# Optimization experiments

Hardware: AMD Instinct MI355X
Metric: run time of the kernel (lower is better)

## Reference

```python
import jax, jax.numpy as jnp
import numpy as np

N_NODES = 20000
N_EDGES = 640000
HIDDEN = 128
NUM_FILTERS = 128
NUM_RBF = 50
NUM_LAYERS = 6
MAX_Z = 100
CUTOFF_UPPER = 5.0
CUTOFF_LOWER = 0.0


def _cosine_cutoff(d):
    # torchmd CosineCutoff with cutoff_lower == 0
    c = 0.5 * (jnp.cos(d * jnp.pi / CUTOFF_UPPER) + 1.0)
    return c * (d < CUTOFF_UPPER).astype(d.dtype)


def setup_inputs() -> dict:
    key = jax.random.key(0)
    ks = jax.random.split(key, 16)
    s = 0.05
    z = jax.random.randint(ks[0], (N_NODES,), 0, MAX_Z)
    pos = jax.random.uniform(ks[1], (N_NODES, 3), dtype=jnp.float32) * 3.0
    src = jax.random.randint(ks[2], (N_EDGES,), 0, N_NODES)
    off = jax.random.randint(ks[3], (N_EDGES,), 1, N_NODES)
    dst = (src + off) % N_NODES  # no self loops -> d > 0 a.s.
    edge_index = jnp.stack([src, dst])
    batch = jnp.zeros((N_NODES,), dtype=jnp.int32)
    # expnorm RBF initial params (ExpNormalSmearing._initial_params)
    start = float(np.exp(-CUTOFF_UPPER + CUTOFF_LOWER))
    rbf_means = jnp.linspace(start, 1.0, NUM_RBF, dtype=jnp.float32)
    rbf_betas = jnp.full((NUM_RBF,), (2.0 / NUM_RBF * (1.0 - start)) ** -2, dtype=jnp.float32)

    def w(k, shape):
        return jax.random.normal(k, shape, dtype=jnp.float32) * s

    L = NUM_LAYERS
    return dict(
        z=z, pos=pos, edge_index=edge_index, batch=batch,
        emb_table=w(ks[4], (MAX_Z, HIDDEN)),
        nbr_emb_table=w(ks[5], (MAX_Z, HIDDEN)),
        nbr_proj_W=w(ks[6], (NUM_RBF, HIDDEN)),
        nbr_proj_b=jnp.zeros((HIDDEN,), jnp.float32),
        combine_W=w(ks[7], (2 * HIDDEN, HIDDEN)),
        combine_b=jnp.zeros((HIDDEN,), jnp.float32),
        rbf_means=rbf_means, rbf_betas=rbf_betas,
        mlp_W1=w(ks[8], (L, NUM_RBF, NUM_FILTERS)),
        mlp_b1=jnp.zeros((L, NUM_FILTERS), jnp.float32),
        mlp_W2=w(ks[9], (L, NUM_FILTERS, NUM_FILTERS)),
        mlp_b2=jnp.zeros((L, NUM_FILTERS), jnp.float32),
        lin1_W=w(ks[10], (L, HIDDEN, NUM_FILTERS)),
        lin2_W=w(ks[11], (L, NUM_FILTERS, HIDDEN)),
        lin2_b=jnp.zeros((L, HIDDEN), jnp.float32),
        lin_W=w(ks[12], (L, HIDDEN, HIDDEN)),
        lin_b=jnp.zeros((L, HIDDEN), jnp.float32),
    )


def reference(z, pos, edge_index, batch, emb_table, nbr_emb_table,
              nbr_proj_W, nbr_proj_b, combine_W, combine_b,
              rbf_means, rbf_betas,
              mlp_W1, mlp_b1, mlp_W2, mlp_b2,
              lin1_W, lin2_W, lin2_b, lin_W, lin_b):
    src, dst = edge_index[0], edge_index[1]
    # Distance (loop=False): edge_vec = pos[src] - pos[dst]
    vec = pos[src] - pos[dst]                      # [E, 3]
    d = jnp.sqrt(jnp.sum(vec * vec, axis=-1))      # [E]
    C = _cosine_cutoff(d)                          # [E]
    alpha = 5.0 / (CUTOFF_UPPER - CUTOFF_LOWER)
    # ExpNormalSmearing: C(d) * exp(-beta * (exp(alpha*(-d+low)) - mu)^2)
    edge_attr = C[:, None] * jnp.exp(
        -rbf_betas * (jnp.exp(alpha * (-d[:, None] + CUTOFF_LOWER)) - rbf_means) ** 2
    )                                              # [E, R]
    x = emb_table[z]                               # [N, H]
    # NeighborEmbedding (self-loop edges masked out, add aggregation)
    nl_mask = (src != dst).astype(x.dtype)
    Wn = (edge_attr @ nbr_proj_W + nbr_proj_b) * (C * nl_mask)[:, None]  # [E, H]
    xn = nbr_emb_table[z]
    agg = jax.ops.segment_sum(xn[src] * Wn, dst, num_segments=N_NODES)
    x = jnp.concatenate([x, agg], axis=1) @ combine_W + combine_b

    def layer(xc, p):
        W1, b1, W2, b2, l1W, l2W, l2b, lW, lb = p
        # CFConv filter: MLP(edge_attr) * cosine_cutoff
        Wf = (jax.nn.silu(edge_attr @ W1 + b1) @ W2 + b2) * C[:, None]   # [E, F]
        h = xc @ l1W                                                      # [N, F]
        ag = jax.ops.segment_sum(h[src] * Wf, dst, num_segments=N_NODES)  # scatter-add
        h = jax.nn.silu(ag @ l2W + l2b)
        h = h @ lW + lb
        return xc + h, None

    x, _ = jax.lax.scan(layer, x, (mlp_W1, mlp_b1, mlp_W2, mlp_b2,
                                   lin1_W, lin2_W, lin2_b, lin_W, lin_b))
    return x
```

## Files before the change

kernel.cpp:

```cpp
#include <hip/hip_runtime.h>
#include <hip/hip_bf16.h>
#include <math.h>

#define NN 20000
#define NE 640000
#define H  128
#define RB 50
#define NL 6
#define TBINS 4096
#define WBLK (128 * 136)

typedef unsigned short u16;
typedef __attribute__((ext_vector_type(8))) short short8v;
typedef __attribute__((ext_vector_type(4))) float f32x4;

__device__ __forceinline__ u16 f2b(float v) {
  unsigned x = __float_as_uint(v);
  unsigned r = (x + 0x7FFFu + ((x >> 16) & 1u)) >> 16;
  return (u16)r;
}
__device__ __forceinline__ float b2f(u16 u) {
  return __uint_as_float(((unsigned int)u) << 16);
}

__global__ void k_hist(const int* __restrict__ ei, int* __restrict__ counts) {
  int e = blockIdx.x * blockDim.x + threadIdx.x;
  if (e < NE) atomicAdd(&counts[ei[NE + e]], 1);
}
__global__ __launch_bounds__(1024) void k_scan(const int* __restrict__ counts,
                                               int* __restrict__ cursor) {
  __shared__ int tsum[1024];
  int tid = threadIdx.x;
  int base = tid * 20;
  int s = 0;
  #pragma unroll
  for (int j = 0; j < 20; ++j) {
    int i = base + j;
    s += (i < NN) ? counts[i] : 0;
  }
  tsum[tid] = s;
  __syncthreads();
  for (int off = 1; off < 1024; off <<= 1) {
    int t = (tid >= off) ? tsum[tid - off] : 0;
    __syncthreads();
    tsum[tid] += t;
    __syncthreads();
  }
  int run = (tid > 0) ? tsum[tid - 1] : 0;
  #pragma unroll
  for (int j = 0; j < 20; ++j) {
    int i = base + j;
    if (i < NN) { cursor[i] = run; run += counts[i]; }
  }
}
__global__ void k_place(const int* __restrict__ ei, int* __restrict__ cursor,
                        int* __restrict__ perm) {
  int e = blockIdx.x * blockDim.x + threadIdx.x;
  if (e < NE) {
    int d = ei[NE + e];
    int p = atomicAdd(&cursor[d], 1);
    perm[p] = e;
  }
}

__global__ void k_edge(const int* __restrict__ ei, const int* __restrict__ perm,
                       const float* __restrict__ pos,
                       int* __restrict__ srcS, float* __restrict__ tvS) {
  int p = blockIdx.x * 256 + threadIdx.x;
  if (p >= NE) return;
  int e = perm[p];
  int s = ei[e], t = ei[NE + e];
  srcS[p] = s;
  float dx = pos[3*s]   - pos[3*t];
  float dy = pos[3*s+1] - pos[3*t+1];
  float dz = pos[3*s+2] - pos[3*t+2];
  float d = sqrtf(dx*dx + dy*dy + dz*dz);
  tvS[p] = expf(-d);
}

__global__ __launch_bounds__(256) void k_tbuild(
    const float* __restrict__ means, const float* __restrict__ betas,
    const float* __restrict__ npW, const float* __restrict__ npb,
    const float* __restrict__ W1, const float* __restrict__ b1,
    const float* __restrict__ W2, const float* __restrict__ b2,
    u16* __restrict__ tb)
{
  int t  = blockIdx.x / (TBINS / 32);
  int j0 = (blockIdx.x % (TBINS / 32)) * 32;
  __shared__ float sAttr[32][52];
  __shared__ float sCut[32];
  __shared__ float sT[32][132];
  int tid = threadIdx.x;
  float tv0 = expf(-5.f);
  float dtv = (1.f - tv0) / (float)(TBINS - 1);
  for (int idx = tid; idx < 32 * RB; idx += 256) {
    int r = idx / RB, k = idx % RB;
    float tv = tv0 + (j0 + r) * dtv;
    float d = -logf(tv);
    float C = 0.5f * (cosf(d * 0.628318530717958647692f) + 1.f);
    if (d >= 5.f) C = 0.f;
    float diff = tv - means[k];
    sAttr[r][k] = C * expf(-betas[k] * diff * diff);
    if (k == 0) sCut[r] = C;
  }
  __syncthreads();
  int g = tid >> 5, c0 = (tid & 31) * 4, eb = g * 4;
  float acc[4][4];
  #pragma unroll
  for (int i = 0; i < 4; ++i)
    for (int j = 0; j < 4; ++j) acc[i][j] = 0.f;
  const float* Wa = (t == 0) ? npW : (W1 + (size_t)(t - 1) * RB * H);
  for (int k = 0; k < RB; ++k) {
    float4 wv = *(const float4*)&Wa[(size_t)k * H + c0];
    #pragma unroll
    for (int i = 0; i < 4; ++i) {
      float a = sAttr[eb + i][k];
      acc[i][0] += a * wv.x; acc[i][1] += a * wv.y;
      acc[i][2] += a * wv.z; acc[i][3] += a * wv.w;
    }
  }
  size_t obase = (size_t)t * TBINS * H;
  int pb = (c0 & 15) * 8 + (c0 >> 4);
  if (t == 0) {
    float4 b4 = *(const float4*)&npb[c0];
    float bvA[4] = {b4.x, b4.y, b4.z, b4.w};
    #pragma unroll
    for (int i = 0; i < 4; ++i) {
      float Cv = sCut[eb + i];
      size_t rb = obase + (size_t)(j0 + eb + i) * H;
      #pragma unroll
      for (int j = 0; j < 4; ++j)
        tb[rb + pb + 8 * j] = f2b((acc[i][j] + bvA[j]) * Cv);
    }
  } else {
    float4 b4 = *(const float4*)&b1[(size_t)(t - 1) * H + c0];
    float bvA[4] = {b4.x, b4.y, b4.z, b4.w};
    #pragma unroll
    for (int i = 0; i < 4; ++i) {
      #pragma unroll
      for (int j = 0; j < 4; ++j) {
        float v = acc[i][j] + bvA[j];
        sT[eb + i][c0 + j] = v / (1.f + __expf(-v));
      }
    }
    __syncthreads();
    #pragma unroll
    for (int i = 0; i < 4; ++i)
      for (int j = 0; j < 4; ++j) acc[i][j] = 0.f;
    const float* Wb = W2 + (size_t)(t - 1) * H * H;
    for (int k = 0; k < H; ++k) {
      float4 wv = *(const float4*)&Wb[(size_t)k * H + c0];
      #pragma unroll
      for (int i = 0; i < 4; ++i) {
        float a = sT[eb + i][k];
        acc[i][0] += a * wv.x; acc[i][1] += a * wv.y;
        acc[i][2] += a * wv.z; acc[i][3] += a * wv.w;
      }
    }
    float4 b24 = *(const float4*)&b2[(size_t)(t - 1) * H + c0];
    float bvB[4] = {b24.x, b24.y, b24.z, b24.w};
    #pragma unroll
    for (int i = 0; i < 4; ++i) {
      float Cv = sCut[eb + i];
      size_t rb = obase + (size_t)(j0 + eb + i) * H;
      #pragma unroll
      for (int j = 0; j < 4; ++j)
        tb[rb + pb + 8 * j] = f2b((acc[i][j] + bvB[j]) * Cv);
    }
  }
}

__global__ void k_prepw2(const float* __restrict__ l2W, const float* __restrict__ lW,
                         const float* __restrict__ l1W, const float* __restrict__ cW,
                         u16* __restrict__ wt) {
  int i = blockIdx.x * 256 + threadIdx.x;
  if (i >= (3 * NL + 2) * WBLK) return;
  if (i < 3 * NL * WBLK) {
    int a = i / (NL * WBLK);
    int r = i % (NL * WBLK);
    int l = r / WBLK;
    int r2 = r % WBLK;
    int n = r2 / 136, k = r2 % 136;
    const float* src = (a == 0) ? l2W : (a == 1) ? lW : l1W;
    wt[i] = (k < H) ? f2b(src[(size_t)l * H * H + (size_t)k * H + n]) : (u16)0;
  } else {
    int j = i - 3 * NL * WBLK;
    int which = j / WBLK;
    int r2 = j % WBLK;
    int n = r2 / 136, k = r2 % 136;
    wt[i] = (k < H) ? f2b(cW[(size_t)(which * 128 + k) * H + n]) : (u16)0;
  }
}

__global__ void k_embed(const int* __restrict__ z, const float* __restrict__ emb,
                        const float* __restrict__ nemb,
                        float* __restrict__ x, u16* __restrict__ xnb) {
  int i = blockIdx.x * blockDim.x + threadIdx.x;
  if (i >= NN * H) return;
  int n = i >> 7, c = i & (H - 1);
  long o = (long)z[n] * H + c;
  x[i] = emb[o];
  xnb[(size_t)n * H + ((c & 15) * 8 + (c >> 4))] = f2b(nemb[o]);
}

__global__ __launch_bounds__(256) void k_eso(
    const int* __restrict__ counts, const int* __restrict__ cursor,
    const int* __restrict__ srcS, const float* __restrict__ tvS,
    const u16* __restrict__ tb, const u16* __restrict__ hsrc,
    float* __restrict__ agg, int maskSelf)
{
  int tid = threadIdx.x;
  int n = blockIdx.x * 16 + (tid >> 4);
  int r16 = tid & 15;
  int cnt = counts[n];
  long e0 = (long)cursor[n] - cnt;
  float tv0 = expf(-5.f);
  float inv = (float)(TBINS - 1) / (1.f - tv0);
  float vsum[8];
  #pragma unroll
  for (int ct = 0; ct < 8; ++ct) vsum[ct] = 0.f;
  int P0_s = 0, P1_s = 0, P2_s = 0;
  float P0_w = 0.f, P1_w = 0.f, P2_w = 0.f;
  short8v P0_hv, P0_lo, P0_hi, P1_hv, P1_lo, P1_hi, P2_hv, P2_lo, P2_hi;
#define ISSUE(P, ii) { int _i = (ii); if (_i < cnt) { \
    long e = e0 + _i; \
    P##_s = srcS[e]; float tvv = tvS[e]; \
    P##_hv = *(const short8v*)&hsrc[(size_t)P##_s * H + r16 * 8]; \
    float u = fminf(fmaxf((tvv - tv0) * inv, 0.f), (float)(TBINS - 1) - 1e-3f); \
    int jj = (int)u; P##_w = u - (float)jj; \
    P##_lo = *(const short8v*)&tb[(size_t)jj * H + r16 * 8]; \
    P##_hi = *(const short8v*)&tb[(size_t)(jj + 1) * H + r16 * 8]; } }
#define CONSUME(P) { \
    float m = (maskSelf && P##_s == n) ? 0.f : 1.f; \
    _Pragma("unroll") \
    for (int ct = 0; ct < 8; ++ct) { \
      float lo = b2f((u16)P##_lo[ct]); \
      float hi = b2f((u16)P##_hi[ct]); \
      vsum[ct] += (lo + P##_w * (hi - lo)) * m * b2f((u16)P##_hv[ct]); \
    } }
  ISSUE(P0, 0); ISSUE(P1, 1); ISSUE(P2, 2);
  for (int i = 0; i < cnt; i += 3) {
    CONSUME(P0); ISSUE(P0, i + 3);
    if (i + 1 < cnt) { CONSUME(P1); ISSUE(P1, i + 4); }
    if (i + 2 < cnt) { CONSUME(P2); ISSUE(P2, i + 5); }
  }
#undef ISSUE
#undef CONSUME
  float* ap = agg + (size_t)n * H + r16;
  #pragma unroll
  for (int ct = 0; ct < 8; ++ct) ap[ct * 16] = vsum[ct];
}

__global__ __launch_bounds__(256) void k_combineM(
    const float* __restrict__ xb, const float* __restrict__ ag,
    const u16* __restrict__ cWt0, const u16* __restrict__ cWt1,
    const float* __restrict__ cb, const u16* __restrict__ l1W0t,
    float* __restrict__ xout, u16* __restrict__ hb)
{
  __shared__ __align__(16) u16 sX[64 * 136];
  __shared__ __align__(16) u16 sG[64 * 136];
  int tid = threadIdx.x;
  int lane = tid & 63, wv = tid >> 6;
  int r16 = lane & 15, g4 = lane >> 4;
  int n0 = blockIdx.x * 64;
  #pragma unroll
  for (int j = 0; j < 8; ++j) {
    int f4 = tid + j * 256;
    int r = f4 >> 5, c4 = f4 & 31;
    int n = n0 + r;
    float4 vx = make_float4(0.f, 0.f, 0.f, 0.f);
    float4 vg = make_float4(0.f, 0.f, 0.f, 0.f);
    if (n < NN) {
      vx = *(const float4*)&xb[(size_t)n * H + c4 * 4];
      vg = *(const float4*)&ag[(size_t)n * H + c4 * 4];
    }
    *(unsigned*)&sX[r * 136 + c4 * 4]     = (unsigned)f2b(vx.x) | ((unsigned)f2b(vx.y) << 16);
    *(unsigned*)&sX[r * 136 + c4 * 4 + 2] = (unsigned)f2b(vx.z) | ((unsigned)f2b(vx.w) << 16);
    *(unsigned*)&sG[r * 136 + c4 * 4]     = (unsigned)f2b(vg.x) | ((unsigned)f2b(vg.y) << 16);
    *(unsigned*)&sG[r * 136 + c4 * 4 + 2] = (unsigned)f2b(vg.z) | ((unsigned)f2b(vg.w) << 16);
  }
  __syncthreads();
  int wrow = wv * 16;
  f32x4 acc[8];
  #pragma unroll
  for (int ct = 0; ct < 8; ++ct) acc[ct] = (f32x4){0.f, 0.f, 0.f, 0.f};
  #pragma unroll
  for (int kt = 0; kt < 4; ++kt) {
    short8v aF = *(const short8v*)&sX[(wrow + r16) * 136 + kt * 32 + g4 * 8];
    #pragma unroll
    for (int ct = 0; ct < 8; ++ct) {
      short8v bF = *(const short8v*)&cWt0[(ct * 16 + r16) * 136 + kt * 32 + g4 * 8];
      acc[ct] = __builtin_amdgcn_mfma_f32_16x16x32_bf16(aF, bF, acc[ct], 0, 0, 0);
    }
  }
  #pragma unroll
  for (int kt = 0; kt < 4; ++kt) {
    short8v aF = *(const short8v*)&sG[(wrow + r16) * 136 + kt * 32 + g4 * 8];
    #pragma unroll
    for (int ct = 0; ct < 8; ++ct) {
      short8v bF = *(const short8v*)&cWt1[(ct * 16 + r16) * 136 + kt * 32 + g4 * 8];
      acc[ct] = __builtin_amdgcn_mfma_f32_16x16x32_bf16(aF, bF, acc[ct], 0, 0, 0);
    }
  }
  #pragma unroll
  for (int ct = 0; ct < 8; ++ct) {
    float bb = cb[ct * 16 + r16];
    #pragma unroll
    for (int r = 0; r < 4; ++r) {
      int n = n0 + wrow + g4 * 4 + r;
      if (n < NN) {
        float o = acc[ct][r] + bb;
        xout[(size_t)n * H + ct * 16 + r16] = o;
        sX[(wrow + g4 * 4 + r) * 136 + ct * 16 + r16] = f2b(o);
      }
    }
  }
  #pragma unroll
  for (int ct = 0; ct < 8; ++ct) acc[ct] = (f32x4){0.f, 0.f, 0.f, 0.f};
  #pragma unroll
  for (int kt = 0; kt < 4; ++kt) {
    short8v aF = *(const short8v*)&sX[(wrow + r16) * 136 + kt * 32 + g4 * 8];
    #pragma unroll
    for (int ct = 0; ct < 8; ++ct) {
      short8v bF = *(const short8v*)&l1W0t[(ct * 16 + r16) * 136 + kt * 32 + g4 * 8];
      acc[ct] = __builtin_amdgcn_mfma_f32_16x16x32_bf16(aF, bF, acc[ct], 0, 0, 0);
    }
  }
  #pragma unroll
  for (int r = 0; r < 4; ++r) {
    int n = n0 + wrow + g4 * 4 + r;
    if (n < NN) {
      short8v hv;
      #pragma unroll
      for (int ct = 0; ct < 8; ++ct) hv[ct] = (short)f2b(acc[ct][r]);
      *(short8v*)&hb[(size_t)n * H + r16 * 8] = hv;
    }
  }
}

__global__ __launch_bounds__(128) void k_gemmM(
    const float* __restrict__ A, const u16* __restrict__ W2t, const float* __restrict__ b2,
    const u16* __restrict__ W3t, const float* __restrict__ b3,
    const float* __restrict__ xin, float* __restrict__ xout,
    const u16* __restrict__ l1Wnt, u16* __restrict__ hb)
{
  __shared__ __align__(16) u16 sA[32 * 136];
  __shared__ __align__(16) u16 sT[32 * 136];
  int tid = threadIdx.x;
  int lane = tid & 63, wv = tid >> 6;
  int r16 = lane & 15, g4 = lane >> 4;
  int n0 = blockIdx.x * 32;
  #pragma unroll
  for (int j = 0; j < 8; ++j) {
    int f4 = tid + j * 128;
    int r = f4 >> 5, c4 = f4 & 31;
    float4 v = *(const float4*)&A[(size_t)(n0 + r) * H + c4 * 4];
    *(unsigned*)&sA[r * 136 + c4 * 4]     = (unsigned)f2b(v.x) | ((unsigned)f2b(v.y) << 16);
    *(unsigned*)&sA[r * 136 + c4 * 4 + 2] = (unsigned)f2b(v.z) | ((unsigned)f2b(v.w) << 16);
  }
  __syncthreads();
  int wrow = wv * 16;
  f32x4 acc[8];
  #pragma unroll
  for (int ct = 0; ct < 8; ++ct) acc[ct] = (f32x4){0.f, 0.f, 0.f, 0.f};
  #pragma unroll
  for (int kt = 0; kt < 4; ++kt) {
    short8v aF = *(const short8v*)&sA[(wrow + r16) * 136 + kt * 32 + g4 * 8];
    #pragma unroll
    for (int ct = 0; ct < 8; ++ct) {
      short8v bF = *(const short8v*)&W2t[(ct * 16 + r16) * 136 + kt * 32 + g4 * 8];
      acc[ct] = __builtin_amdgcn_mfma_f32_16x16x32_bf16(aF, bF, acc[ct], 0, 0, 0);
    }
  }
  #pragma unroll
  for (int ct = 0; ct < 8; ++ct) {
    float bb = b2[ct * 16 + r16];
    #pragma unroll
    for (int r = 0; r < 4; ++r) {
      float v = acc[ct][r] + bb;
      v = v / (1.f + __expf(-v));
      sT[(wrow + g4 * 4 + r) * 136 + ct * 16 + r16] = f2b(v);
    }
  }
  #pragma unroll
  for (int ct = 0; ct < 8; ++ct) acc[ct] = (f32x4){0.f, 0.f, 0.f, 0.f};
  #pragma unroll
  for (int kt = 0; kt < 4; ++kt) {
    short8v aF = *(const short8v*)&sT[(wrow + r16) * 136 + kt * 32 + g4 * 8];
    #pragma unroll
    for (int ct = 0; ct < 8; ++ct) {
      short8v bF = *(const short8v*)&W3t[(ct * 16 + r16) * 136 + kt * 32 + g4 * 8];
      acc[ct] = __builtin_amdgcn_mfma_f32_16x16x32_bf16(aF, bF, acc[ct], 0, 0, 0);
    }
  }
  #pragma unroll
  for (int ct = 0; ct < 8; ++ct) {
    float bb = b3[ct * 16 + r16];
    #pragma unroll
    for (int r = 0; r < 4; ++r) {
      int n = n0 + wrow + g4 * 4 + r;
      float o = acc[ct][r] + bb + xin[(size_t)n * H + ct * 16 + r16];
      xout[(size_t)n * H + ct * 16 + r16] = o;
      sA[(wrow + g4 * 4 + r) * 136 + ct * 16 + r16] = f2b(o);
    }
  }
  if (!l1Wnt) return;
  #pragma unroll
  for (int ct = 0; ct < 8; ++ct) acc[ct] = (f32x4){0.f, 0.f, 0.f, 0.f};
  #pragma unroll
  for (int kt = 0; kt < 4; ++kt) {
    short8v aF = *(const short8v*)&sA[(wrow + r16) * 136 + kt * 32 + g4 * 8];
    #pragma unroll
    for (int ct = 0; ct < 8; ++ct) {
      short8v bF = *(const short8v*)&l1Wnt[(ct * 16 + r16) * 136 + kt * 32 + g4 * 8];
      acc[ct] = __builtin_amdgcn_mfma_f32_16x16x32_bf16(aF, bF, acc[ct], 0, 0, 0);
    }
  }
  #pragma unroll
  for (int r = 0; r < 4; ++r) {
    int n = n0 + wrow + g4 * 4 + r;
    short8v hv;
    #pragma unroll
    for (int ct = 0; ct < 8; ++ct) hv[ct] = (short)f2b(acc[ct][r]);
    *(short8v*)&hb[(size_t)n * H + r16 * 8] = hv;
  }
}

extern "C" void kernel_launch(void* const* d_in, const int* in_sizes, int n_in,
                              void* d_out, int out_size, void* d_ws, size_t ws_size,
                              hipStream_t stream) {
  int bo = (n_in >= 4 && in_sizes[3] == NN) ? 0 : -1;
  const int*   z     = (const int*)d_in[0];
  const float* pos   = (const float*)d_in[1];
  const int*   ei    = (const int*)d_in[2];
  const float* emb   = (const float*)d_in[4 + bo];
  const float* nemb  = (const float*)d_in[5 + bo];
  const float* npW   = (const float*)d_in[6 + bo];
  const float* npb   = (const float*)d_in[7 + bo];
  const float* cW    = (const float*)d_in[8 + bo];
  const float* cb    = (const float*)d_in[9 + bo];
  const float* means = (const float*)d_in[10 + bo];
  const float* betas = (const float*)d_in[11 + bo];
  const float* W1    = (const float*)d_in[12 + bo];
  const float* b1    = (const float*)d_in[13 + bo];
  const float* W2    = (const float*)d_in[14 + bo];
  const float* b2    = (const float*)d_in[15 + bo];
  const float* l1W   = (const float*)d_in[16 + bo];
  const float* l2W   = (const float*)d_in[17 + bo];
  const float* l2b   = (const float*)d_in[18 + bo];
  const float* lW    = (const float*)d_in[19 + bo];
  const float* lb    = (const float*)d_in[20 + bo];

  char* w = (char*)d_ws;
  auto alloc = [&](size_t bytes) { char* p = w; w += (bytes + 255) & ~(size_t)255; return p; };
  int*   counts = (int*)  alloc((size_t)NN * 4);
  int*   cursor = (int*)  alloc((size_t)NN * 4);
  int*   perm   = (int*)  alloc((size_t)NE * 4);
  int*   srcS   = (int*)  alloc((size_t)NE * 4);
  float* tvS    = (float*)alloc((size_t)NE * 4);
  u16*   tb     = (u16*)  alloc((size_t)7 * TBINS * H * 2);
  u16*   wt     = (u16*)  alloc((size_t)(3 * NL + 2) * WBLK * 2);
  float* xbuf   = (float*)alloc((size_t)NN * H * 4);
  float* agg    = (float*)alloc((size_t)NN * H * 4);
  u16*   xnb    = (u16*)  alloc((size_t)NN * H * 2);
  u16*   hbA    = (u16*)  alloc((size_t)NN * H * 2);
  u16*   hbB    = (u16*)  alloc((size_t)NN * H * 2);

  u16* l2Wt = wt;
  u16* lWt  = wt + (size_t)NL * WBLK;
  u16* l1Wt = wt + (size_t)2 * NL * WBLK;
  u16* cWt0 = wt + (size_t)3 * NL * WBLK;
  u16* cWt1 = cWt0 + WBLK;

  dim3 b256(256);
  int gE256 = (NE + 255) / 256;
  int gNH   = (NN * H + 255) / 256;
  int gESO  = NN / 16;
  int gC    = (NN + 63) / 64;
  int gM    = NN / 32;
  int gTB   = 7 * (TBINS / 32);
  int gPW   = ((3 * NL + 2) * WBLK + 255) / 256;

  hipMemsetAsync(counts, 0, (size_t)NN * 4, stream);
  k_hist<<<gE256, b256, 0, stream>>>(ei, counts);
  k_scan<<<1, 1024, 0, stream>>>(counts, cursor);
  k_place<<<gE256, b256, 0, stream>>>(ei, cursor, perm);
  k_edge<<<gE256, b256, 0, stream>>>(ei, perm, pos, srcS, tvS);
  k_tbuild<<<gTB, b256, 0, stream>>>(means, betas, npW, npb, W1, b1, W2, b2, tb);
  k_prepw2<<<gPW, b256, 0, stream>>>(l2W, lW, l1W, cW, wt);
  k_embed<<<gNH, b256, 0, stream>>>(z, emb, nemb, xbuf, xnb);

  k_eso<<<gESO, b256, 0, stream>>>(counts, cursor, srcS, tvS, tb, xnb, agg, 1);
  k_combineM<<<gC, b256, 0, stream>>>(xbuf, agg, cWt0, cWt1, cb, l1Wt, xbuf, hbA);

  u16* hin = hbA;
  u16* hout = hbB;
  for (int l = 0; l < NL; ++l) {
    k_eso<<<gESO, b256, 0, stream>>>(counts, cursor, srcS, tvS,
                                     tb + (size_t)(1 + l) * TBINS * H,
                                     hin, agg, 0);
    const u16* l1Wnt = (l + 1 < NL) ? (l1Wt + (size_t)(l + 1) * WBLK) : nullptr;
    float* xo = (l == NL - 1) ? (float*)d_out : xbuf;
    k_gemmM<<<gM, dim3(128), 0, stream>>>(agg, l2Wt + (size_t)l * WBLK, l2b + (size_t)l * H,
                                          lWt + (size_t)l * WBLK, lb + (size_t)l * H,
                                          xbuf, xo, l1Wnt, hout);
    u16* tmp = hin; hin = hout; hout = tmp;
  }
}
```

Before: 561.5 us.

## Pad per-node edge lists to multiples of three and pair table rows

Each node's CSR segment is padded to a multiple of three. Pad slots get src 0 and tv=exp(-5), which gives a zero cutoff and so a zero contribution. This lets the k_eso gather loop drop its per-edge bounds checks. The filter table is stored with each bin's row interleaved with the next bin's row, so one 32-byte load fetches both interpolation endpoints. The separate perm and edge kernels are merged into one atomic placement kernel. In exchange the table doubles in size, padding adds extra edge work and a fill kernel, and correctness depends on the cutoff making pad entries exactly zero.

```diff
diff --git a/kernel.cpp b/kernel.cpp
--- a/kernel.cpp
+++ b/kernel.cpp
@@ -9,6 +9,7 @@
 #define NL 6
 #define TBINS 4096
 #define WBLK (128 * 136)
+#define NEPAD (NE + 2 * NN + 64)
 
 typedef unsigned short u16;
 typedef __attribute__((ext_vector_type(8))) short short8v;
@@ -28,7 +29,8 @@
   if (e < NE) atomicAdd(&counts[ei[NE + e]], 1);
 }
 __global__ __launch_bounds__(1024) void k_scan(const int* __restrict__ counts,
-                                               int* __restrict__ cursor) {
+                                               int* __restrict__ pstart,
+                                               int* __restrict__ cursorP) {
   __shared__ int tsum[1024];
   int tid = threadIdx.x;
   int base = tid * 20;
@@ -36,7 +38,7 @@
   #pragma unroll
   for (int j = 0; j < 20; ++j) {
     int i = base + j;
-    s += (i < NN) ? counts[i] : 0;
+    if (i < NN) { int c = counts[i]; s += ((c + 2) / 3) * 3; }
   }
   tsum[tid] = s;
   __syncthreads();
@@ -50,31 +52,29 @@
   #pragma unroll
   for (int j = 0; j < 20; ++j) {
     int i = base + j;
-    if (i < NN) { cursor[i] = run; run += counts[i]; }
-  }
-}
-__global__ void k_place(const int* __restrict__ ei, int* __restrict__ cursor,
-                        int* __restrict__ perm) {
+    if (i < NN) {
+      pstart[i] = run; cursorP[i] = run;
+      int c = counts[i];
+      run += ((c + 2) / 3) * 3;
+    }
+  }
+}
+__global__ void k_fill(int* __restrict__ srcS, float* __restrict__ tvS) {
+  int i = blockIdx.x * blockDim.x + threadIdx.x;
+  if (i < NEPAD) { srcS[i] = 0; tvS[i] = expf(-5.f); }
+}
+__global__ void k_placeE(const int* __restrict__ ei, const float* __restrict__ pos,
+                         int* __restrict__ cursorP,
+                         int* __restrict__ srcS, float* __restrict__ tvS) {
   int e = blockIdx.x * blockDim.x + threadIdx.x;
-  if (e < NE) {
-    int d = ei[NE + e];
-    int p = atomicAdd(&cursor[d], 1);
-    perm[p] = e;
-  }
-}
-
-__global__ void k_edge(const int* __restrict__ ei, const int* __restrict__ perm,
-                       const float* __restrict__ pos,
-                       int* __restrict__ srcS, float* __restrict__ tvS) {
-  int p = blockIdx.x * 256 + threadIdx.x;
-  if (p >= NE) return;
-  int e = perm[p];
+  if (e >= NE) return;
   int s = ei[e], t = ei[NE + e];
-  srcS[p] = s;
+  int p = atomicAdd(&cursorP[t], 1);
   float dx = pos[3*s]   - pos[3*t];
   float dy = pos[3*s+1] - pos[3*t+1];
   float dz = pos[3*s+2] - pos[3*t+2];
   float d = sqrtf(dx*dx + dy*dy + dz*dz);
+  srcS[p] = s;
   tvS[p] = expf(-d);
 }
 
@@ -83,7 +83,7 @@
     const float* __restrict__ npW, const float* __restrict__ npb,
     const float* __restrict__ W1, const float* __restrict__ b1,
     const float* __restrict__ W2, const float* __restrict__ b2,
-    u16* __restrict__ tb)
+    u16* __restrict__ tbp)
 {
   int t  = blockIdx.x / (TBINS / 32);
   int j0 = (blockIdx.x % (TBINS / 32)) * 32;
@@ -119,18 +119,16 @@
       acc[i][2] += a * wv.z; acc[i][3] += a * wv.w;
     }
   }
-  size_t obase = (size_t)t * TBINS * H;
-  int pb = (c0 & 15) * 8 + (c0 >> 4);
+  size_t obase = (size_t)t * TBINS * 256;
+  float fout[4][4];
   if (t == 0) {
     float4 b4 = *(const float4*)&npb[c0];
     float bvA[4] = {b4.x, b4.y, b4.z, b4.w};
     #pragma unroll
     for (int i = 0; i < 4; ++i) {
       float Cv = sCut[eb + i];
-      size_t rb = obase + (size_t)(j0 + eb + i) * H;
       #pragma unroll
-      for (int j = 0; j < 4; ++j)
-        tb[rb + pb + 8 * j] = f2b((acc[i][j] + bvA[j]) * Cv);
+      for (int j = 0; j < 4; ++j) fout[i][j] = (acc[i][j] + bvA[j]) * Cv;
     }
   } else {
     float4 b4 = *(const float4*)&b1[(size_t)(t - 1) * H + c0];
@@ -162,10 +160,21 @@
     #pragma unroll
     for (int i = 0; i < 4; ++i) {
       float Cv = sCut[eb + i];
-      size_t rb = obase + (size_t)(j0 + eb + i) * H;
       #pragma unroll
-      for (int j = 0; j < 4; ++j)
-        tb[rb + pb + 8 * j] = f2b((acc[i][j] + bvB[j]) * Cv);
+      for (int j = 0; j < 4; ++j) fout[i][j] = (acc[i][j] + bvB[j]) * Cv;
+    }
+  }
+  #pragma unroll
+  for (int i = 0; i < 4; ++i) {
+    int jrow = j0 + eb + i;
+    #pragma unroll
+    for (int j = 0; j < 4; ++j) {
+      int c = c0 + j;
+      u16 v = f2b(fout[i][j]);
+      int g16 = c & 15, slot = c >> 4;
+      tbp[obase + ((size_t)jrow * 16 + g16) * 16 + slot] = v;
+      if (jrow >= 1)
+        tbp[obase + ((size_t)(jrow - 1) * 16 + g16) * 16 + 8 + slot] = v;
     }
   }
 }
@@ -204,32 +213,34 @@
 }
 
 __global__ __launch_bounds__(256) void k_eso(
-    const int* __restrict__ counts, const int* __restrict__ cursor,
+    const int* __restrict__ counts, const int* __restrict__ pstart,
     const int* __restrict__ srcS, const float* __restrict__ tvS,
-    const u16* __restrict__ tb, const u16* __restrict__ hsrc,
+    const u16* __restrict__ tbp, const u16* __restrict__ hsrc,
     float* __restrict__ agg, int maskSelf)
 {
   int tid = threadIdx.x;
   int n = blockIdx.x * 16 + (tid >> 4);
   int r16 = tid & 15;
   int cnt = counts[n];
-  long e0 = (long)cursor[n] - cnt;
+  int cntp = ((cnt + 2) / 3) * 3;
+  long e0 = (long)pstart[n];
   float tv0 = expf(-5.f);
   float inv = (float)(TBINS - 1) / (1.f - tv0);
   float vsum[8];
   #pragma unroll
   for (int ct = 0; ct < 8; ++ct) vsum[ct] = 0.f;
-  int P0_s = 0, P1_s = 0, P2_s = 0;
-  float P0_w = 0.f, P1_w = 0.f, P2_w = 0.f;
+  int P0_s, P1_s, P2_s;
+  float P0_w, P1_w, P2_w;
   short8v P0_hv, P0_lo, P0_hi, P1_hv, P1_lo, P1_hi, P2_hv, P2_lo, P2_hi;
-#define ISSUE(P, ii) { int _i = (ii); if (_i < cnt) { \
-    long e = e0 + _i; \
+#define ISSUE(P, ii) { \
+    long e = e0 + (ii); \
     P##_s = srcS[e]; float tvv = tvS[e]; \
     P##_hv = *(const short8v*)&hsrc[(size_t)P##_s * H + r16 * 8]; \
     float u = fminf(fmaxf((tvv - tv0) * inv, 0.f), (float)(TBINS - 1) - 1e-3f); \
     int jj = (int)u; P##_w = u - (float)jj; \
-    P##_lo = *(const short8v*)&tb[(size_t)jj * H + r16 * 8]; \
-    P##_hi = *(const short8v*)&tb[(size_t)(jj + 1) * H + r16 * 8]; } }
+    const u16* tp = &tbp[((size_t)jj * 16 + r16) * 16]; \
+    P##_lo = *(const short8v*)tp; \
+    P##_hi = *(const short8v*)(tp + 8); }
 #define CONSUME(P) { \
     float m = (maskSelf && P##_s == n) ? 0.f : 1.f; \
     _Pragma("unroll") \
@@ -239,10 +250,10 @@
       vsum[ct] += (lo + P##_w * (hi - lo)) * m * b2f((u16)P##_hv[ct]); \
     } }
   ISSUE(P0, 0); ISSUE(P1, 1); ISSUE(P2, 2);
-  for (int i = 0; i < cnt; i += 3) {
+  for (int i = 0; i < cntp; i += 3) {
     CONSUME(P0); ISSUE(P0, i + 3);
-    if (i + 1 < cnt) { CONSUME(P1); ISSUE(P1, i + 4); }
-    if (i + 2 < cnt) { CONSUME(P2); ISSUE(P2, i + 5); }
+    CONSUME(P1); ISSUE(P1, i + 4);
+    CONSUME(P2); ISSUE(P2, i + 5);
   }
 #undef ISSUE
 #undef CONSUME
@@ -453,18 +464,18 @@
 
   char* w = (char*)d_ws;
   auto alloc = [&](size_t bytes) { char* p = w; w += (bytes + 255) & ~(size_t)255; return p; };
-  int*   counts = (int*)  alloc((size_t)NN * 4);
-  int*   cursor = (int*)  alloc((size_t)NN * 4);
-  int*   perm   = (int*)  alloc((size_t)NE * 4);
-  int*   srcS   = (int*)  alloc((size_t)NE * 4);
-  float* tvS    = (float*)alloc((size_t)NE * 4);
-  u16*   tb     = (u16*)  alloc((size_t)7 * TBINS * H * 2);
-  u16*   wt     = (u16*)  alloc((size_t)(3 * NL + 2) * WBLK * 2);
-  float* xbuf   = (float*)alloc((size_t)NN * H * 4);
-  float* agg    = (float*)alloc((size_t)NN * H * 4);
-  u16*   xnb    = (u16*)  alloc((size_t)NN * H * 2);
-  u16*   hbA    = (u16*)  alloc((size_t)NN * H * 2);
-  u16*   hbB    = (u16*)  alloc((size_t)NN * H * 2);
+  int*   counts  = (int*)  alloc((size_t)NN * 4);
+  int*   pstart  = (int*)  alloc((size_t)NN * 4);
+  int*   cursorP = (int*)  alloc((size_t)NN * 4);
+  int*   srcS    = (int*)  alloc((size_t)NEPAD * 4);
+  float* tvS     = (float*)alloc((size_t)NEPAD * 4);
+  u16*   tbp     = (u16*)  alloc((size_t)7 * TBINS * 256 * 2);
+  u16*   wt      = (u16*)  alloc((size_t)(3 * NL + 2) * WBLK * 2);
+  float* xbuf    = (float*)alloc((size_t)NN * H * 4);
+  float* agg     = (float*)alloc((size_t)NN * H * 4);
+  u16*   xnb     = (u16*)  alloc((size_t)NN * H * 2);
+  u16*   hbA     = (u16*)  alloc((size_t)NN * H * 2);
+  u16*   hbB     = (u16*)  alloc((size_t)NN * H * 2);
 
   u16* l2Wt = wt;
   u16* lWt  = wt + (size_t)NL * WBLK;
@@ -475,6 +486,7 @@
   dim3 b256(256);
   int gE256 = (NE + 255) / 256;
   int gNH   = (NN * H + 255) / 256;
+  int gFILL = (NEPAD + 255) / 256;
   int gESO  = NN / 16;
   int gC    = (NN + 63) / 64;
   int gM    = NN / 32;
@@ -483,21 +495,21 @@
 
   hipMemsetAsync(counts, 0, (size_t)NN * 4, stream);
   k_hist<<<gE256, b256, 0, stream>>>(ei, counts);
-  k_scan<<<1, 1024, 0, stream>>>(counts, cursor);
-  k_place<<<gE256, b256, 0, stream>>>(ei, cursor, perm);
-  k_edge<<<gE256, b256, 0, stream>>>(ei, perm, pos, srcS, tvS);
-  k_tbuild<<<gTB, b256, 0, stream>>>(means, betas, npW, npb, W1, b1, W2, b2, tb);
+  k_scan<<<1, 1024, 0, stream>>>(counts, pstart, cursorP);
+  k_fill<<<gFILL, b256, 0, stream>>>(srcS, tvS);
+  k_placeE<<<gE256, b256, 0, stream>>>(ei, pos, cursorP, srcS, tvS);
+  k_tbuild<<<gTB, b256, 0, stream>>>(means, betas, npW, npb, W1, b1, W2, b2, tbp);
   k_prepw2<<<gPW, b256, 0, stream>>>(l2W, lW, l1W, cW, wt);
   k_embed<<<gNH, b256, 0, stream>>>(z, emb, nemb, xbuf, xnb);
 
-  k_eso<<<gESO, b256, 0, stream>>>(counts, cursor, srcS, tvS, tb, xnb, agg, 1);
+  k_eso<<<gESO, b256, 0, stream>>>(counts, pstart, srcS, tvS, tbp, xnb, agg, 1);
   k_combineM<<<gC, b256, 0, stream>>>(xbuf, agg, cWt0, cWt1, cb, l1Wt, xbuf, hbA);
 
   u16* hin = hbA;
   u16* hout = hbB;
   for (int l = 0; l < NL; ++l) {
-    k_eso<<<gESO, b256, 0, stream>>>(counts, cursor, srcS, tvS,
-                                     tb + (size_t)(1 + l) * TBINS * H,
+    k_eso<<<gESO, b256, 0, stream>>>(counts, pstart, srcS, tvS,
+                                     tbp + (size_t)(1 + l) * TBINS * 256,
                                      hin, agg, 0);
     const u16* l1Wnt = (l + 1 < NL) ? (l1Wt + (size_t)(l + 1) * WBLK) : nullptr;
     float* xo = (l == NL - 1) ? (float*)d_out : xbuf;
```

Result: slower. 582.1 us (+3.7%).
